# Performance work log

Hardware: AMD Instinct MI355X
Metric: run time of the kernel (lower is better)

Reference implementation:

```python
import jax, jax.numpy as jnp
import numpy as np

DISP_W, MAT_W, CD_W = 1.0, 0.1, 0.5
CHUNK = 512


def _min_dists(a, b):
    # a: [B, Na, 3], b: [B, Nb, 3] -> per-point min squared distance [B, Na]
    B, Na, _ = a.shape
    a_chunks = jnp.swapaxes(a.reshape(B, Na // CHUNK, CHUNK, 3), 0, 1)  # [nc, B, chunk, 3]

    def body(carry, ac):  # ac: [B, chunk, 3]
        d = jnp.sum((ac[:, :, None, :] - b[:, None, :, :]) ** 2, axis=-1)  # [B, chunk, Nb]
        return carry, jnp.min(d, axis=-1)

    _, mins = jax.lax.scan(body, 0, a_chunks)  # [nc, B, chunk]
    return jnp.moveaxis(mins, 0, 1).reshape(B, Na)


def chamfer_distance(pred, target):
    min_p2t = _min_dists(pred, target)
    min_t2p = _min_dists(target, pred)
    return (min_p2t.mean(axis=1) + min_t2p.mean(axis=1)).mean()


def setup_inputs() -> dict:
    key = jax.random.key(0)
    k1, k2, k3, k4, k5 = jax.random.split(key, 5)
    B, N = 4, 8192
    return {
        "pred_disp": jax.random.normal(k1, (B, N, 3), dtype=jnp.float32),
        "pred_mat": jax.random.normal(k2, (B, 2), dtype=jnp.float32),
        "target_disp": jax.random.normal(k3, (B, N, 3), dtype=jnp.float32),
        "target_mat": jax.random.normal(k4, (B, 2), dtype=jnp.float32),
        "template": jax.random.normal(k5, (B, N, 3), dtype=jnp.float32),
    }


def reference(pred_disp, pred_mat, target_disp, target_mat, template):
    disp_loss = jnp.mean(jnp.abs(pred_disp - target_disp))
    mat_loss = jnp.mean((pred_mat - target_mat) ** 2)
    pred_pos = template + pred_disp
    target_pos = template + target_disp
    cd = chamfer_distance(pred_pos, target_pos)
    total = DISP_W * disp_loss + MAT_W * mat_loss + CD_W * cd
    return total
```

## Files before the change

### kernel.cpp

```cpp
#include <hip/hip_runtime.h>

#define DISP_W 1.0f
#define MAT_W  0.1f
#define CD_W   0.5f

typedef _Float16 half8 __attribute__((ext_vector_type(8)));
typedef float f32x16 __attribute__((ext_vector_type(16)));
typedef float f32x4  __attribute__((ext_vector_type(4)));

constexpr int BB = 4;
constexpr int NN = 8192;
constexpr int THREADS = 256;
constexpr int IB = 256;
constexpr int JR = 1024;
constexpr int NIB = NN / IB;
constexpr int NJB = NN / JR;
constexpr int NCHUNK = JR / 32;
constexpr int NPTS = 2 * BB * NN;
constexpr int GRID = 2 * BB * NIB * NJB;
constexpr int RSTRIDE = 36;


__global__ __launch_bounds__(256)
void build_frags(const float* __restrict__ pred_disp,
                 const float* __restrict__ target_disp,
                 const float* __restrict__ tmpl,
                 half8* __restrict__ fragA,
                 half8* __restrict__ fragBhi,
                 half8* __restrict__ fragBlo,
                 float* __restrict__ out)
{
    int p = blockIdx.x * 256 + threadIdx.x;
    if (p == 0) out[0] = 0.0f;
    int c = p >> 15;
    int b = (p >> 13) & (BB - 1);
    int n = p & (NN - 1);

    const float* dp = (c ? target_disp : pred_disp) + (size_t)b * NN * 3;
    const float* tp = tmpl + (size_t)b * NN * 3;

    int n3 = n * 3;
    float x = tp[n3 + 0] + dp[n3 + 0];
    float y = tp[n3 + 1] + dp[n3 + 1];
    float z = tp[n3 + 2] + dp[n3 + 2];
    float cc = fmaf(x, x, fmaf(y, y, z * z));

    _Float16 xh = (_Float16)x;  _Float16 xl = (_Float16)(x - (float)xh);
    _Float16 yh = (_Float16)y;  _Float16 yl = (_Float16)(y - (float)yh);
    _Float16 zh = (_Float16)z;  _Float16 zl = (_Float16)(z - (float)zh);
    _Float16 ch = (_Float16)cc; _Float16 cl = (_Float16)(cc - (float)ch);

    float ux = -2.0f * x, uy = -2.0f * y, uz = -2.0f * z;
    _Float16 uxh = (_Float16)ux; _Float16 uxl = (_Float16)(ux - (float)uxh);
    _Float16 uyh = (_Float16)uy; _Float16 uyl = (_Float16)(uy - (float)uyh);
    _Float16 uzh = (_Float16)uz; _Float16 uzl = (_Float16)(uz - (float)uzh);

    const _Float16 one  = (_Float16)1.0f;
    const _Float16 zero = (_Float16)0.0f;

    half8 aHi = {xh, yh, zh, xh, yh, zh, xl, yl};
    half8 aLo = {zl, ch, cl, one, one, zero, zero, zero};
    half8 bHi = {uxh, uyh, uzh, uxl, uyl, uzl, uxh, uyh};
    half8 bLo = {uzh, one, one, ch, cl, zero, zero, zero};

    fragA[(size_t)p * 2 + 0] = aHi;
    fragA[(size_t)p * 2 + 1] = aLo;
    fragBhi[p] = bHi;
    fragBlo[p] = bLo;
}

__global__ __launch_bounds__(THREADS, 2)
void chamfer_mfma(const half8* __restrict__ fragA,
                  const half8* __restrict__ fragBhi,
                  const half8* __restrict__ fragBlo,
                  float* __restrict__ rowpart)
{
    __shared__ __align__(16) char lds_raw[32768];
    half8* sBhi = (half8*)lds_raw;
    half8* sBlo = (half8*)(lds_raw + 16384);

    int bx = blockIdx.x;
    int jBlk = bx & (NJB - 1);
    int iBlk = (bx >> 3) & (NIB - 1);
    int b    = (bx >> 8) & (BB - 1);
    int dir  = bx >> 10;
    int cA = dir, cB = dir ^ 1;

    const int tid  = threadIdx.x;
    const int lane = tid & 63;
    const int w    = tid >> 6;
    const int hi   = lane >> 5;
    const int li   = lane & 31;

    size_t pB = ((size_t)cB * BB + b) * NN + (size_t)jBlk * JR;
    const half8* gHi = fragBhi + pB;
    const half8* gLo = fragBlo + pB;
    #pragma unroll
    for (int t = 0; t < JR / THREADS; ++t) {
        int idx = t * THREADS + tid;
        sBhi[idx] = gHi[idx];
        sBlo[idx] = gLo[idx];
    }

    int i0 = iBlk * IB + w * 64 + li;
    size_t aBase = ((size_t)cA * BB + b) * NN;
    half8 aF0 = fragA[(aBase + i0) * 2 + hi];
    half8 aF1 = fragA[(aBase + i0 + 32) * 2 + hi];

    __syncthreads();

    f32x16 kZero = {0.f,0.f,0.f,0.f, 0.f,0.f,0.f,0.f, 0.f,0.f,0.f,0.f, 0.f,0.f,0.f,0.f};
    const half8* baseB = hi ? sBlo : sBhi;
    float rm0[16], rm1[16];
    #pragma unroll
    for (int r = 0; r < 16; ++r) { rm0[r] = 1.0e30f; rm1[r] = 1.0e30f; }

    #pragma unroll 4
    for (int c = 0; c < NCHUNK; ++c) {
        half8 b0 = baseB[c * 32 + li];
        f32x16 a0 = __builtin_amdgcn_mfma_f32_32x32x16_f16(aF0, b0, kZero, 0, 0, 0);
        f32x16 a1 = __builtin_amdgcn_mfma_f32_32x32x16_f16(aF1, b0, kZero, 0, 0, 0);
        #pragma unroll
        for (int r = 0; r < 16; ++r)
            rm0[r] = fminf(rm0[r], a0[r]);
        #pragma unroll
        for (int r = 0; r < 16; ++r)
            rm1[r] = fminf(rm1[r], a1[r]);
    }

    __syncthreads();
    float* scr = (float*)lds_raw;
    int wbase = w * (32 * RSTRIDE);
    int cbase = wbase + hi * 4 * RSTRIDE + li;
    size_t obase = ((size_t)(dir * BB + b) * NJB + jBlk) * NN
                 + (size_t)iBlk * IB + w * 64;

    #pragma unroll
    for (int r = 0; r < 16; ++r)
        scr[cbase + ((r & 3) + 8 * (r >> 2)) * RSTRIDE] = rm0[r];
    __syncthreads();
    {
        const f32x4* rp = (const f32x4*)&scr[wbase + (lane & 31) * RSTRIDE];
        f32x4 q0 = rp[0], q1 = rp[1], q2 = rp[2], q3 = rp[3];
        f32x4 q4 = rp[4], q5 = rp[5], q6 = rp[6], q7 = rp[7];
        f32x4 m4;
        #pragma unroll
        for (int k = 0; k < 4; ++k)
            m4[k] = fminf(fminf(fminf(q0[k], q1[k]), fminf(q2[k], q3[k])),
                          fminf(fminf(q4[k], q5[k]), fminf(q6[k], q7[k])));
        float m = fminf(fminf(m4[0], m4[1]), fminf(m4[2], m4[3]));
        if (lane < 32) rowpart[obase + lane] = m;
    }
    __syncthreads();

    #pragma unroll
    for (int r = 0; r < 16; ++r)
        scr[cbase + ((r & 3) + 8 * (r >> 2)) * RSTRIDE] = rm1[r];
    __syncthreads();
    {
        const f32x4* rp = (const f32x4*)&scr[wbase + (lane & 31) * RSTRIDE];
        f32x4 q0 = rp[0], q1 = rp[1], q2 = rp[2], q3 = rp[3];
        f32x4 q4 = rp[4], q5 = rp[5], q6 = rp[6], q7 = rp[7];
        f32x4 m4;
        #pragma unroll
        for (int k = 0; k < 4; ++k)
            m4[k] = fminf(fminf(fminf(q0[k], q1[k]), fminf(q2[k], q3[k])),
                          fminf(fminf(q4[k], q5[k]), fminf(q6[k], q7[k])));
        float m = fminf(fminf(m4[0], m4[1]), fminf(m4[2], m4[3]));
        if (lane < 32) rowpart[obase + 32 + lane] = m;
    }
}

__global__ __launch_bounds__(256)
void final_reduce(const float* __restrict__ pred_disp,
                  const float* __restrict__ target_disp,
                  const float* __restrict__ pred_mat,
                  const float* __restrict__ target_mat,
                  const float* __restrict__ rowpart,
                  float* __restrict__ out)
{
    const int NDISP = BB * NN * 3;
    const int NROWS = 2 * BB * NN;

    int gtid = blockIdx.x * blockDim.x + threadIdx.x;
    int gstride = gridDim.x * blockDim.x;

    float dsum = 0.0f;
    for (int i = gtid; i < NDISP; i += gstride)
        dsum += fabsf(pred_disp[i] - target_disp[i]);

    float msum = 0.0f;
    for (int t = gtid; t < NROWS; t += gstride) {
        int db = t >> 13;
        int i  = t & (NN - 1);
        const float* p = rowpart + (size_t)db * NJB * NN + i;
        float m = 1.0e30f;
        #pragma unroll
        for (int jb = 0; jb < NJB; ++jb)
            m = fminf(m, p[(size_t)jb * NN]);
        msum += fmaxf(m, 0.0f);
    }

    float acc = dsum * (DISP_W / (float)NDISP)
              + msum * (CD_W / (float)(BB * NN));

    if (gtid < 2 * BB) {
        float d = pred_mat[gtid] - target_mat[gtid];
        acc += d * d * (MAT_W / (float)(2 * BB));
    }

    for (int off = 32; off > 0; off >>= 1)
        acc += __shfl_down(acc, off, 64);

    __shared__ float wsum[4];
    if ((threadIdx.x & 63) == 0) wsum[threadIdx.x >> 6] = acc;
    __syncthreads();
    if (threadIdx.x == 0)
        atomicAdd(out, wsum[0] + wsum[1] + wsum[2] + wsum[3]);
}

extern "C" void kernel_launch(void* const* d_in, const int* in_sizes, int n_in,
                              void* d_out, int out_size, void* d_ws, size_t ws_size,
                              hipStream_t stream) {
    const float* pred_disp   = (const float*)d_in[0];
    const float* pred_mat    = (const float*)d_in[1];
    const float* target_disp = (const float*)d_in[2];
    const float* target_mat  = (const float*)d_in[3];
    const float* tmpl        = (const float*)d_in[4];

    half8* fragA   = (half8*)d_ws;
    half8* fragBhi = fragA + (size_t)NPTS * 2;
    half8* fragBlo = fragBhi + NPTS;
    float* rowpart = (float*)(fragBlo + NPTS);
    float* out = (float*)d_out;

    build_frags<<<NPTS / 256, 256, 0, stream>>>(pred_disp, target_disp, tmpl,
                                                fragA, fragBhi, fragBlo, out);
    chamfer_mfma<<<GRID, THREADS, 0, stream>>>(fragA, fragBhi, fragBlo, rowpart);
    final_reduce<<<256, 256, 0, stream>>>(pred_disp, target_disp, pred_mat, target_mat,
                                          rowpart, out);
}
```

Measured before the change: 35.58 us.

## Loop two j-stages per block and fuse L1 disp sum into frag build

Each chamfer block now walks two consecutive 1024-point B tiles, reusing its loaded A fragments and halving the grid and the rowpart partial-min buffer. The final reduce then takes a min over four partials instead of eight. The absolute displacement sum moves into build_frags as per-block partials, so final_reduce no longer rereads both displacement arrays. The output zeroing becomes a hipMemsetAsync. The cost is fewer blocks (1024 instead of 2048) and an extra sync per stage with no overlap between tile loads and MFMA work.

```diff
diff --git a/kernel.cpp b/kernel.cpp
--- a/kernel.cpp
+++ b/kernel.cpp
@@ -13,12 +13,14 @@
 constexpr int THREADS = 256;
 constexpr int IB = 256;
 constexpr int JR = 1024;
+constexpr int NSTAGE = 2;
 constexpr int NIB = NN / IB;
-constexpr int NJB = NN / JR;
+constexpr int NJQ = NN / (JR * NSTAGE);
 constexpr int NCHUNK = JR / 32;
 constexpr int NPTS = 2 * BB * NN;
-constexpr int GRID = 2 * BB * NIB * NJB;
+constexpr int GRID = 2 * BB * NIB * NJQ;
 constexpr int RSTRIDE = 36;
+constexpr int NBF = NPTS / 256;
 
 
 __global__ __launch_bounds__(256)
@@ -28,10 +30,9 @@
                  half8* __restrict__ fragA,
                  half8* __restrict__ fragBhi,
                  half8* __restrict__ fragBlo,
-                 float* __restrict__ out)
+                 float* __restrict__ dsum_ws)
 {
     int p = blockIdx.x * 256 + threadIdx.x;
-    if (p == 0) out[0] = 0.0f;
     int c = p >> 15;
     int b = (p >> 13) & (BB - 1);
     int n = p & (NN - 1);
@@ -40,10 +41,17 @@
     const float* tp = tmpl + (size_t)b * NN * 3;
 
     int n3 = n * 3;
-    float x = tp[n3 + 0] + dp[n3 + 0];
-    float y = tp[n3 + 1] + dp[n3 + 1];
-    float z = tp[n3 + 2] + dp[n3 + 2];
+    float dx = dp[n3 + 0], dy = dp[n3 + 1], dz = dp[n3 + 2];
+    float x = tp[n3 + 0] + dx;
+    float y = tp[n3 + 1] + dy;
+    float z = tp[n3 + 2] + dz;
     float cc = fmaf(x, x, fmaf(y, y, z * z));
+
+    float s = 0.0f;
+    if (c == 0) {
+        const float* td = target_disp + (size_t)b * NN * 3;
+        s = fabsf(dx - td[n3 + 0]) + fabsf(dy - td[n3 + 1]) + fabsf(dz - td[n3 + 2]);
+    }
 
     _Float16 xh = (_Float16)x;  _Float16 xl = (_Float16)(x - (float)xh);
     _Float16 yh = (_Float16)y;  _Float16 yl = (_Float16)(y - (float)yh);
@@ -67,6 +75,15 @@
     fragA[(size_t)p * 2 + 1] = aLo;
     fragBhi[p] = bHi;
     fragBlo[p] = bLo;
+
+    for (int off = 32; off > 0; off >>= 1)
+        s += __shfl_down(s, off, 64);
+    __shared__ float ws4[4];
+    int lane = threadIdx.x & 63, w = threadIdx.x >> 6;
+    if (lane == 0) ws4[w] = s;
+    __syncthreads();
+    if (threadIdx.x == 0)
+        dsum_ws[blockIdx.x] = ws4[0] + ws4[1] + ws4[2] + ws4[3];
 }
 
 __global__ __launch_bounds__(THREADS, 2)
@@ -80,10 +97,10 @@
     half8* sBlo = (half8*)(lds_raw + 16384);
 
     int bx = blockIdx.x;
-    int jBlk = bx & (NJB - 1);
-    int iBlk = (bx >> 3) & (NIB - 1);
-    int b    = (bx >> 8) & (BB - 1);
-    int dir  = bx >> 10;
+    int jq   = bx & (NJQ - 1);
+    int iBlk = (bx >> 2) & (NIB - 1);
+    int b    = (bx >> 7) & (BB - 1);
+    int dir  = bx >> 9;
     int cA = dir, cB = dir ^ 1;
 
     const int tid  = threadIdx.x;
@@ -92,47 +109,51 @@
     const int hi   = lane >> 5;
     const int li   = lane & 31;
 
-    size_t pB = ((size_t)cB * BB + b) * NN + (size_t)jBlk * JR;
-    const half8* gHi = fragBhi + pB;
-    const half8* gLo = fragBlo + pB;
-    #pragma unroll
-    for (int t = 0; t < JR / THREADS; ++t) {
-        int idx = t * THREADS + tid;
-        sBhi[idx] = gHi[idx];
-        sBlo[idx] = gLo[idx];
-    }
-
     int i0 = iBlk * IB + w * 64 + li;
     size_t aBase = ((size_t)cA * BB + b) * NN;
     half8 aF0 = fragA[(aBase + i0) * 2 + hi];
     half8 aF1 = fragA[(aBase + i0 + 32) * 2 + hi];
 
-    __syncthreads();
+    size_t pB = ((size_t)cB * BB + b) * NN + (size_t)jq * (JR * NSTAGE);
+    const half8* gHi = fragBhi + pB;
+    const half8* gLo = fragBlo + pB;
 
     f32x16 kZero = {0.f,0.f,0.f,0.f, 0.f,0.f,0.f,0.f, 0.f,0.f,0.f,0.f, 0.f,0.f,0.f,0.f};
-    const half8* baseB = hi ? sBlo : sBhi;
     float rm0[16], rm1[16];
     #pragma unroll
     for (int r = 0; r < 16; ++r) { rm0[r] = 1.0e30f; rm1[r] = 1.0e30f; }
 
-    #pragma unroll 4
-    for (int c = 0; c < NCHUNK; ++c) {
-        half8 b0 = baseB[c * 32 + li];
-        f32x16 a0 = __builtin_amdgcn_mfma_f32_32x32x16_f16(aF0, b0, kZero, 0, 0, 0);
-        f32x16 a1 = __builtin_amdgcn_mfma_f32_32x32x16_f16(aF1, b0, kZero, 0, 0, 0);
+    for (int s = 0; s < NSTAGE; ++s) {
+        const half8* srcHi = gHi + (size_t)s * JR;
+        const half8* srcLo = gLo + (size_t)s * JR;
         #pragma unroll
-        for (int r = 0; r < 16; ++r)
-            rm0[r] = fminf(rm0[r], a0[r]);
-        #pragma unroll
-        for (int r = 0; r < 16; ++r)
-            rm1[r] = fminf(rm1[r], a1[r]);
-    }
-
-    __syncthreads();
+        for (int t = 0; t < JR / THREADS; ++t) {
+            int idx = t * THREADS + tid;
+            sBhi[idx] = srcHi[idx];
+            sBlo[idx] = srcLo[idx];
+        }
+        __syncthreads();
+
+        const half8* baseB = hi ? sBlo : sBhi;
+        #pragma unroll 4
+        for (int c = 0; c < NCHUNK; ++c) {
+            half8 b0 = baseB[c * 32 + li];
+            f32x16 a0 = __builtin_amdgcn_mfma_f32_32x32x16_f16(aF0, b0, kZero, 0, 0, 0);
+            f32x16 a1 = __builtin_amdgcn_mfma_f32_32x32x16_f16(aF1, b0, kZero, 0, 0, 0);
+            #pragma unroll
+            for (int r = 0; r < 16; ++r)
+                rm0[r] = fminf(rm0[r], a0[r]);
+            #pragma unroll
+            for (int r = 0; r < 16; ++r)
+                rm1[r] = fminf(rm1[r], a1[r]);
+        }
+        __syncthreads();
+    }
+
     float* scr = (float*)lds_raw;
     int wbase = w * (32 * RSTRIDE);
     int cbase = wbase + hi * 4 * RSTRIDE + li;
-    size_t obase = ((size_t)(dir * BB + b) * NJB + jBlk) * NN
+    size_t obase = ((size_t)(dir * BB + b) * NJQ + jq) * NN
                  + (size_t)iBlk * IB + w * 64;
 
     #pragma unroll
@@ -172,37 +193,31 @@
 }
 
 __global__ __launch_bounds__(256)
-void final_reduce(const float* __restrict__ pred_disp,
-                  const float* __restrict__ target_disp,
-                  const float* __restrict__ pred_mat,
+void final_reduce(const float* __restrict__ pred_mat,
                   const float* __restrict__ target_mat,
                   const float* __restrict__ rowpart,
+                  const float* __restrict__ dsum_ws,
                   float* __restrict__ out)
 {
-    const int NDISP = BB * NN * 3;
     const int NROWS = 2 * BB * NN;
 
     int gtid = blockIdx.x * blockDim.x + threadIdx.x;
     int gstride = gridDim.x * blockDim.x;
-
-    float dsum = 0.0f;
-    for (int i = gtid; i < NDISP; i += gstride)
-        dsum += fabsf(pred_disp[i] - target_disp[i]);
 
     float msum = 0.0f;
     for (int t = gtid; t < NROWS; t += gstride) {
         int db = t >> 13;
         int i  = t & (NN - 1);
-        const float* p = rowpart + (size_t)db * NJB * NN + i;
-        float m = 1.0e30f;
-        #pragma unroll
-        for (int jb = 0; jb < NJB; ++jb)
-            m = fminf(m, p[(size_t)jb * NN]);
+        const float* p = rowpart + (size_t)db * NJQ * NN + i;
+        float m = fminf(fminf(p[0], p[(size_t)NN]),
+                        fminf(p[(size_t)2 * NN], p[(size_t)3 * NN]));
         msum += fmaxf(m, 0.0f);
     }
 
-    float acc = dsum * (DISP_W / (float)NDISP)
-              + msum * (CD_W / (float)(BB * NN));
+    float acc = msum * (CD_W / (float)(BB * NN));
+
+    if (gtid < NBF)
+        acc += dsum_ws[gtid] * (DISP_W / (float)(BB * NN * 3));
 
     if (gtid < 2 * BB) {
         float d = pred_mat[gtid] - target_mat[gtid];
@@ -232,11 +247,13 @@
     half8* fragBhi = fragA + (size_t)NPTS * 2;
     half8* fragBlo = fragBhi + NPTS;
     float* rowpart = (float*)(fragBlo + NPTS);
+    float* dsum_ws = rowpart + (size_t)2 * BB * NJQ * NN;
     float* out = (float*)d_out;
 
-    build_frags<<<NPTS / 256, 256, 0, stream>>>(pred_disp, target_disp, tmpl,
-                                                fragA, fragBhi, fragBlo, out);
+    hipMemsetAsync(d_out, 0, sizeof(float), stream);
+
+    build_frags<<<NBF, 256, 0, stream>>>(pred_disp, target_disp, tmpl,
+                                         fragA, fragBhi, fragBlo, dsum_ws);
     chamfer_mfma<<<GRID, THREADS, 0, stream>>>(fragA, fragBhi, fragBlo, rowpart);
-    final_reduce<<<256, 256, 0, stream>>>(pred_disp, target_disp, pred_mat, target_mat,
-                                          rowpart, out);
-}
+    final_reduce<<<128, 256, 0, stream>>>(pred_mat, target_mat, rowpart, dsum_ws, out);
+}
```

New measurement: 36.51 us. 2.6% more time.
